# Optimization experiments

Measured on AMD Instinct MI355X. Metric: run time of the kernel, lower is better.

Reference implementation:

```python
import jax, jax.numpy as jnp
import numpy as np
from jax import lax

EPS = 1e-05
DN = ('NHWC', 'HWIO', 'NHWC')


def setup_inputs() -> dict:
    key = jax.random.key(0)
    k1, k2, k3 = jax.random.split(key, 3)
    x = jax.random.normal(k1, (16, 64, 64, 128), dtype=jnp.float32)
    kernel = jax.random.normal(k2, (3, 3, 128, 256), dtype=jnp.float32) * 0.05
    bias = jax.random.normal(k3, (256,), dtype=jnp.float32) * 0.01
    alpha = jnp.ones((1,), dtype=jnp.float32)
    return {"x": x, "kernel": kernel, "bias": bias, "alpha": alpha}


def reference(x, kernel, bias, alpha):
    # dot-product conv: <patch, W> per output channel  -> [B,H,W,O]
    dot = lax.conv_general_dilated(x, kernel, (1, 1), 'SAME', dimension_numbers=DN)
    # per-patch squared norm ||x_patch||^2 via conv of x^2 with ones kernel -> [B,H,W,1]
    ones_k = jnp.ones(kernel.shape[:-1] + (1,), dtype=x.dtype)
    patch_sq = lax.conv_general_dilated(x * x, ones_k, (1, 1), 'SAME', dimension_numbers=DN)
    # per-output-channel squared kernel norm ||W_o||^2 -> [O]
    kernel_sq = jnp.sum(kernel * kernel, axis=(0, 1, 2))
    # ||x - W||^2 = ||x||^2 - 2<x,W> + ||W||^2
    dist_sq = patch_sq - 2.0 * dot + kernel_sq
    y = (dot * dot) / (dist_sq + EPS)
    y = y + bias
    out_features = kernel.shape[-1]
    scale = (jnp.sqrt(jnp.float32(out_features)) / jnp.log1p(jnp.float32(out_features))) ** alpha
    return y * scale
```

## Files before the change

kernel.cpp:

```cpp
#include <hip/hip_runtime.h>
#include <stdint.h>


#define NB 16
#define HH 64
#define WW 64
#define CC 128
#define OO 256
#define HP 66
#define WP 66
#define KTOT 1152
#define EPSV 1e-5f

typedef short short8 __attribute__((ext_vector_type(8)));
typedef float f32x4 __attribute__((ext_vector_type(4)));

__device__ __forceinline__ unsigned short f2bf(float f) {
  unsigned u = __builtin_bit_cast(unsigned, f);
  u += 0x7fffu + ((u >> 16) & 1u);
  return (unsigned short)(u >> 16);
}

__device__ __forceinline__ void gload_lds16(const void* g, void* l) {
  __builtin_amdgcn_global_load_lds(
      (const __attribute__((address_space(1))) unsigned int*)g,
      (__attribute__((address_space(3))) unsigned int*)l,
      16, 0, 0);
}

__global__ __launch_bounds__(256) void prep_x(const float* __restrict__ x,
                                              unsigned short* __restrict__ xp,
                                              float* __restrict__ s2p) {
  int gw = (blockIdx.x << 2) + (threadIdx.x >> 6);
  int lane = threadIdx.x & 63;
  int b = gw / (HP * WP);
  int rem = gw - b * (HP * WP);
  int hp = rem / WP;
  int wp = rem - hp * WP;
  float2 v = make_float2(0.f, 0.f);
  if (hp >= 1 && hp <= HH && wp >= 1 && wp <= WW) {
    const float2* src = (const float2*)(x + (size_t)(((b * HH) + hp - 1) * WW + (wp - 1)) * CC);
    v = src[lane];
  }
  ushort2 o2;
  o2.x = f2bf(v.x);
  o2.y = f2bf(v.y);
  ((ushort2*)(xp + (size_t)gw * CC))[lane] = o2;
  float ss = v.x * v.x + v.y * v.y;
  #pragma unroll
  for (int off = 32; off > 0; off >>= 1) ss += __shfl_down(ss, off);
  if (lane == 0) s2p[gw] = ss;
}

__global__ __launch_bounds__(256) void prep_w(const float* __restrict__ kern,
                                              unsigned short* __restrict__ wt,
                                              float* __restrict__ ksq) {
  int o = blockIdx.x;
  int t = threadIdx.x;
  float acc = 0.f;
  for (int k = t; k < KTOT; k += 256) {
    float v = kern[(size_t)k * OO + o];
    wt[(size_t)o * KTOT + k] = f2bf(v);
    acc += v * v;
  }
  __shared__ float red[256];
  red[t] = acc;
  __syncthreads();
  #pragma unroll
  for (int s = 128; s > 0; s >>= 1) {
    if (t < s) red[t] += red[t + s];
    __syncthreads();
  }
  if (t == 0) ksq[o] = red[0];
}

__global__ __launch_bounds__(256) void yat_main(
    const unsigned short* __restrict__ xp,
    const unsigned short* __restrict__ wt,
    const float* __restrict__ s2p,
    const float* __restrict__ ksq,
    const float* __restrict__ bias,
    const float* __restrict__ alpha,
    float* __restrict__ out) {
  __shared__ unsigned short As[128 * 32];
  __shared__ unsigned short Bs[128 * 32];
  __shared__ float ps[128];

  int bid = blockIdx.x;
  int swz = ((bid & 7) << 7) + (bid >> 3);
  int mt = swz >> 1;
  int nt = swz & 1;
  int m0 = mt << 7;
  int n0 = nt << 7;

  int tid = threadIdx.x;
  int wid = tid >> 6;
  int lane = tid & 63;

  int r0 = (wid << 4) + (lane >> 2);
  int csub = (lane & 3) << 3;

  const unsigned short* aSrc0;
  const unsigned short* aSrc1;
  {
    int p = m0 + r0;
    int b = p >> 12, hw = p & 4095;
    int h = hw >> 6, w = hw & 63;
    aSrc0 = xp + (size_t)((b * HP + h + 1) * WP + (w + 1)) * CC + csub;
    p = m0 + 64 + r0;
    b = p >> 12; hw = p & 4095; h = hw >> 6; w = hw & 63;
    aSrc1 = xp + (size_t)((b * HP + h + 1) * WP + (w + 1)) * CC + csub;
  }
  const unsigned short* bSrc0 = wt + (size_t)(n0 + r0) * KTOT + csub;
  const unsigned short* bSrc1 = wt + (size_t)(n0 + 64 + r0) * KTOT + csub;

  unsigned short* aDst0 = As + (wid << 9);
  unsigned short* aDst1 = As + 2048 + (wid << 9);
  unsigned short* bDst0 = Bs + (wid << 9);
  unsigned short* bDst1 = Bs + 2048 + (wid << 9);

  int wr = wid >> 1;
  int wc = wid & 1;
  int aOff = ((wr << 6) + (lane & 15)) * 64 + ((lane >> 4) << 4);
  int bOff = ((wc << 6) + (lane & 15)) * 64 + ((lane >> 4) << 4);

  f32x4 acc[4][4] = {};

  #pragma unroll
  for (int dy = 0; dy < 3; ++dy) {
    #pragma unroll
    for (int dx = 0; dx < 3; ++dx) {
      const int aTap = (dy * WP + dx - (WP + 1)) * CC;
      const int bTap = (dy * 3 + dx) * CC;
      #pragma unroll
      for (int c4 = 0; c4 < 4; ++c4) {
        const int coff = c4 << 5;
        __syncthreads();
        gload_lds16(aSrc0 + aTap + coff, aDst0);
        gload_lds16(aSrc1 + aTap + coff, aDst1);
        gload_lds16(bSrc0 + bTap + coff, bDst0);
        gload_lds16(bSrc1 + bTap + coff, bDst1);
        __syncthreads();
        short8 af[4], bf[4];
        #pragma unroll
        for (int m = 0; m < 4; ++m)
          af[m] = *(const short8*)((const char*)As + aOff + (m << 10));
        #pragma unroll
        for (int n = 0; n < 4; ++n)
          bf[n] = *(const short8*)((const char*)Bs + bOff + (n << 10));
        #pragma unroll
        for (int m = 0; m < 4; ++m) {
          #pragma unroll
          for (int n = 0; n < 4; ++n)
            acc[m][n] = __builtin_amdgcn_mfma_f32_16x16x32_bf16(af[m], bf[n], acc[m][n], 0, 0, 0);
        }
      }
    }
  }

  __syncthreads();
  if (tid < 128) {
    int p = m0 + tid;
    int b = p >> 12, hw = p & 4095;
    int h = hw >> 6, w = hw & 63;
    const float* s2 = s2p + (b * HP + h) * WP + w;
    float s = 0.f;
    #pragma unroll
    for (int dy = 0; dy < 3; ++dy) {
      #pragma unroll
      for (int dx = 0; dx < 3; ++dx) s += s2[dy * WP + dx];
    }
    ps[tid] = s;
  }
  __syncthreads();

  float al = alpha[0];
  float scale = powf(16.0f / logf(257.0f), al);

  int c0 = n0 + (wc << 6) + (lane & 15);
  int rb = (wr << 6) + ((lane >> 4) << 2);
  #pragma unroll
  for (int n = 0; n < 4; ++n) {
    int cn = c0 + (n << 4);
    float kq = ksq[cn] + EPSV;
    float bv = bias[cn];
    #pragma unroll
    for (int m = 0; m < 4; ++m) {
      f32x4 a = acc[m][n];
      #pragma unroll
      for (int j = 0; j < 4; ++j) {
        int rm = rb + (m << 4) + j;
        float dot = a[j];
        float dist = ps[rm] - 2.0f * dot + kq;
        float y = dot * dot / dist + bv;
        out[(size_t)(m0 + rm) * OO + cn] = y * scale;
      }
    }
  }
}

extern "C" void kernel_launch(void* const* d_in, const int* in_sizes, int n_in,
                              void* d_out, int out_size, void* d_ws, size_t ws_size,
                              hipStream_t stream) {
  const float* x = (const float*)d_in[0];
  const float* kern = (const float*)d_in[1];
  const float* bias = (const float*)d_in[2];
  const float* alpha = (const float*)d_in[3];
  float* out = (float*)d_out;

  char* ws = (char*)d_ws;
  unsigned short* xp  = (unsigned short*)ws;
  unsigned short* wtb = (unsigned short*)(ws + 17842176);
  float* s2p = (float*)(ws + 18432000);
  float* ksq = (float*)(ws + 18710784);

  prep_x<<<17424, 256, 0, stream>>>(x, xp, s2p);
  prep_w<<<256, 256, 0, stream>>>(kern, wtb, ksq);
  yat_main<<<1024, 256, 0, stream>>>(xp, wtb, s2p, ksq, bias, alpha, out);
}
```

Measured before the change: 156.5 us.

## Pipeline conv GEMM with triple-buffered LDS, larger tiles and XOR swizzle

Reworks the main implicit-GEMM kernel to use 256x128 output tiles with 512 threads, K steps of 64, and a three-slot LDS ring filled by async global-to-LDS loads two stages ahead, with explicit vmcnt waits instead of full sync per step. LDS columns are XOR-swizzled to avoid bank conflicts, and MFMA sections run at raised wave priority. The aim is to hide global load latency behind MFMA work and cut barrier overhead. In exchange it uses about 145KB of dynamic LDS, which limits occupancy, and hand-tuned waitcnt counts that must exactly match the number of loads issued per stage.

```diff
diff --git a/kernel.cpp b/kernel.cpp
--- a/kernel.cpp
+++ b/kernel.cpp
@@ -2,7 +2,6 @@
 #include <stdint.h>
 
 
-#define NB 16
 #define HH 64
 #define WW 64
 #define CC 128
@@ -10,7 +9,14 @@
 #define HP 66
 #define WP 66
 #define KTOT 1152
+#define NKT 18
 #define EPSV 1e-5f
+
+#define BM 256
+#define BN 128
+#define SLOT_BYTES 49152
+#define B_OFF 32768
+#define SMEM_TOTAL (3 * SLOT_BYTES + 1024)
 
 typedef short short8 __attribute__((ext_vector_type(8)));
 typedef float f32x4 __attribute__((ext_vector_type(4)));
@@ -27,6 +33,9 @@
       (__attribute__((address_space(3))) unsigned int*)l,
       16, 0, 0);
 }
+
+#define FENCE() asm volatile("" ::: "memory")
+#define BAR() do { FENCE(); __builtin_amdgcn_s_barrier(); FENCE(); } while (0)
 
 __global__ __launch_bounds__(256) void prep_x(const float* __restrict__ x,
                                               unsigned short* __restrict__ xp,
@@ -74,7 +83,7 @@
   if (t == 0) ksq[o] = red[0];
 }
 
-__global__ __launch_bounds__(256) void yat_main(
+__global__ __launch_bounds__(512, 2) void yat_main(
     const unsigned short* __restrict__ xp,
     const unsigned short* __restrict__ wt,
     const float* __restrict__ s2p,
@@ -82,87 +91,106 @@
     const float* __restrict__ bias,
     const float* __restrict__ alpha,
     float* __restrict__ out) {
-  __shared__ unsigned short As[128 * 32];
-  __shared__ unsigned short Bs[128 * 32];
-  __shared__ float ps[128];
+  extern __shared__ char smem[];
+
+  int tid = threadIdx.x;
+  int wid = tid >> 6, lane = tid & 63;
 
   int bid = blockIdx.x;
-  int swz = ((bid & 7) << 7) + (bid >> 3);
-  int mt = swz >> 1;
-  int nt = swz & 1;
-  int m0 = mt << 7;
+  int swz = ((bid & 7) << 6) + (bid >> 3);
+  int mt = swz >> 1, nt = swz & 1;
+  int m0 = mt << 8;
   int n0 = nt << 7;
 
-  int tid = threadIdx.x;
-  int wid = tid >> 6;
-  int lane = tid & 63;
-
-  int r0 = (wid << 4) + (lane >> 2);
-  int csub = (lane & 3) << 3;
-
-  const unsigned short* aSrc0;
-  const unsigned short* aSrc1;
-  {
-    int p = m0 + r0;
-    int b = p >> 12, hw = p & 4095;
-    int h = hw >> 6, w = hw & 63;
-    aSrc0 = xp + (size_t)((b * HP + h + 1) * WP + (w + 1)) * CC + csub;
-    p = m0 + 64 + r0;
-    b = p >> 12; hw = p & 4095; h = hw >> 6; w = hw & 63;
-    aSrc1 = xp + (size_t)((b * HP + h + 1) * WP + (w + 1)) * CC + csub;
-  }
-  const unsigned short* bSrc0 = wt + (size_t)(n0 + r0) * KTOT + csub;
-  const unsigned short* bSrc1 = wt + (size_t)(n0 + 64 + r0) * KTOT + csub;
-
-  unsigned short* aDst0 = As + (wid << 9);
-  unsigned short* aDst1 = As + 2048 + (wid << 9);
-  unsigned short* bDst0 = Bs + (wid << 9);
-  unsigned short* bDst1 = Bs + 2048 + (wid << 9);
-
-  int wr = wid >> 1;
-  int wc = wid & 1;
-  int aOff = ((wr << 6) + (lane & 15)) * 64 + ((lane >> 4) << 4);
-  int bOff = ((wc << 6) + (lane & 15)) * 64 + ((lane >> 4) << 4);
+  int cg = (((tid & 7) ^ ((tid >> 3) & 7)) << 3);
+  const unsigned short* aSrc[4];
+  #pragma unroll
+  for (int q = 0; q < 4; ++q) {
+    int r = (q << 6) + (tid >> 3);
+    int p = m0 + r;
+    int b = p >> 12, h = (p >> 6) & 63, w = p & 63;
+    aSrc[q] = xp + (size_t)((b * HP + h) * WP + w) * CC + cg;
+  }
+  const unsigned short* bSrc[2];
+  #pragma unroll
+  for (int q = 0; q < 2; ++q) {
+    int r = (q << 6) + (tid >> 3);
+    bSrc[q] = wt + (size_t)(n0 + r) * KTOT + cg;
+  }
+
+  auto STAGE = [&](int t, int soff) {
+    int tap = t >> 1;
+    int dy = tap / 3;
+    int dx = tap - dy * 3;
+    int koff = (dy * WP + dx) * CC + ((t & 1) << 6);
+    char* da = smem + soff + (wid << 10);
+    #pragma unroll
+    for (int q = 0; q < 4; ++q)
+      gload_lds16(aSrc[q] + koff, da + (q << 13));
+    int kb = t << 6;
+    char* db = smem + soff + B_OFF + (wid << 10);
+    #pragma unroll
+    for (int q = 0; q < 2; ++q)
+      gload_lds16(bSrc[q] + kb, db + (q << 13));
+  };
+
+  int wr = wid >> 1, wcn = wid & 1;
+  int rA0 = (wr << 6) + (lane & 15);
+  int rB0 = (wcn << 6) + (lane & 15);
+  int xsw = lane & 7;
+  int co0 = (((lane >> 4) ^ xsw) << 4);
+  int co1 = ((((lane >> 4) + 4) ^ xsw) << 4);
 
   f32x4 acc[4][4] = {};
 
-  #pragma unroll
-  for (int dy = 0; dy < 3; ++dy) {
-    #pragma unroll
-    for (int dx = 0; dx < 3; ++dx) {
-      const int aTap = (dy * WP + dx - (WP + 1)) * CC;
-      const int bTap = (dy * 3 + dx) * CC;
-      #pragma unroll
-      for (int c4 = 0; c4 < 4; ++c4) {
-        const int coff = c4 << 5;
-        __syncthreads();
-        gload_lds16(aSrc0 + aTap + coff, aDst0);
-        gload_lds16(aSrc1 + aTap + coff, aDst1);
-        gload_lds16(bSrc0 + bTap + coff, bDst0);
-        gload_lds16(bSrc1 + bTap + coff, bDst1);
-        __syncthreads();
-        short8 af[4], bf[4];
-        #pragma unroll
-        for (int m = 0; m < 4; ++m)
-          af[m] = *(const short8*)((const char*)As + aOff + (m << 10));
+  STAGE(0, 0);
+  STAGE(1, SLOT_BYTES);
+
+  int soff = 0;
+  int stoff = 2 * SLOT_BYTES;
+  for (int i = 0; i < NKT; ++i) {
+    if (i < NKT - 2) STAGE(i + 2, stoff);
+    if (i < NKT - 2)      asm volatile("s_waitcnt vmcnt(12)" ::: "memory");
+    else if (i == NKT - 2) asm volatile("s_waitcnt vmcnt(6)" ::: "memory");
+    else                   asm volatile("s_waitcnt vmcnt(0)" ::: "memory");
+    BAR();
+
+    const char* Ab = smem + soff;
+    const char* Bb = Ab + B_OFF;
+    short8 af[2][4], bf[2][4];
+    #pragma unroll
+    for (int ks = 0; ks < 2; ++ks) {
+      int co = ks ? co1 : co0;
+      #pragma unroll
+      for (int m = 0; m < 4; ++m)
+        af[ks][m] = *(const short8*)(Ab + ((rA0 + (m << 4)) << 7) + co);
+      #pragma unroll
+      for (int n = 0; n < 4; ++n)
+        bf[ks][n] = *(const short8*)(Bb + ((rB0 + (n << 4)) << 7) + co);
+    }
+    asm volatile("s_waitcnt lgkmcnt(0)" ::: "memory");
+    BAR();
+
+    __builtin_amdgcn_s_setprio(1);
+    #pragma unroll
+    for (int ks = 0; ks < 2; ++ks) {
+      #pragma unroll
+      for (int m = 0; m < 4; ++m) {
         #pragma unroll
         for (int n = 0; n < 4; ++n)
-          bf[n] = *(const short8*)((const char*)Bs + bOff + (n << 10));
-        #pragma unroll
-        for (int m = 0; m < 4; ++m) {
-          #pragma unroll
-          for (int n = 0; n < 4; ++n)
-            acc[m][n] = __builtin_amdgcn_mfma_f32_16x16x32_bf16(af[m], bf[n], acc[m][n], 0, 0, 0);
-        }
+          acc[m][n] = __builtin_amdgcn_mfma_f32_16x16x32_bf16(af[ks][m], bf[ks][n], acc[m][n], 0, 0, 0);
       }
     }
-  }
-
-  __syncthreads();
-  if (tid < 128) {
+    __builtin_amdgcn_s_setprio(0);
+
+    soff += SLOT_BYTES;  if (soff == 3 * SLOT_BYTES) soff = 0;
+    stoff += SLOT_BYTES; if (stoff == 3 * SLOT_BYTES) stoff = 0;
+  }
+
+  float* ps = (float*)(smem + 3 * SLOT_BYTES);
+  if (tid < BM) {
     int p = m0 + tid;
-    int b = p >> 12, hw = p & 4095;
-    int h = hw >> 6, w = hw & 63;
+    int b = p >> 12, h = (p >> 6) & 63, w = p & 63;
     const float* s2 = s2p + (b * HP + h) * WP + w;
     float s = 0.f;
     #pragma unroll
@@ -172,12 +200,13 @@
     }
     ps[tid] = s;
   }
-  __syncthreads();
+  asm volatile("s_waitcnt lgkmcnt(0)" ::: "memory");
+  BAR();
 
   float al = alpha[0];
   float scale = powf(16.0f / logf(257.0f), al);
 
-  int c0 = n0 + (wc << 6) + (lane & 15);
+  int c0 = n0 + (wcn << 6) + (lane & 15);
   int rb = (wr << 6) + ((lane >> 4) << 2);
   #pragma unroll
   for (int n = 0; n < 4; ++n) {
@@ -214,7 +243,10 @@
   float* s2p = (float*)(ws + 18432000);
   float* ksq = (float*)(ws + 18710784);
 
+  (void)hipFuncSetAttribute((const void*)yat_main,
+                            hipFuncAttributeMaxDynamicSharedMemorySize, SMEM_TOTAL);
+
   prep_x<<<17424, 256, 0, stream>>>(x, xp, s2p);
   prep_w<<<256, 256, 0, stream>>>(kern, wtb, ksq);
-  yat_main<<<1024, 256, 0, stream>>>(xp, wtb, s2p, ksq, bias, alpha, out);
-}
+  yat_main<<<512, 512, SMEM_TOTAL, stream>>>(xp, wtb, s2p, ksq, bias, alpha, out);
+}
```

Measured after the change: 149.9 us. 1.04x faster.
